# Kernel optimization log

Measured on AMD Instinct MI355X. Metric: run time of the kernel, lower is better.

The kernel has to match this reference:

```python
import jax, jax.numpy as jnp
import numpy as np

KSIZE = 20      # gaussian smoothing kernel size
SIGMA = 2.0     # gaussianSmoothWidth
STRIDE = 4      # strideLen
KLEN = 14       # kernelLen
LN_EPS = 1e-5


def _gauss_smooth(x):
    # x: [B, T, D]; depthwise conv1d along time, padding='same' (torch: left 9, right 10)
    D = x.shape[-1]
    i = jnp.arange(KSIZE, dtype=x.dtype)
    g = jnp.exp(-0.5 * ((i - (KSIZE - 1) / 2.0) / SIGMA) ** 2)
    g = g / jnp.sum(g)
    k = jnp.tile(g[None, None, :], (D, 1, 1))  # [D, 1, KSIZE]
    y = jax.lax.conv_general_dilated(
        jnp.swapaxes(x, 1, 2), k,
        window_strides=(1,), padding=[(9, 10)],
        feature_group_count=D,
        dimension_numbers=('NCW', 'OIW', 'NCW'))
    return jnp.swapaxes(y, 1, 2)


def _qrnn_layer(x, W, b):
    # SpeechBrain QuasiRNNLayer (output_gate=True, unidirectional, zoneout=0)
    # x: [B, T, F]; W: [3H, 2F]; b: [3H]
    xprev = jnp.concatenate([jnp.zeros_like(x[:, :1]), x[:, :-1]], axis=1)
    y = jnp.einsum('btf,gf->btg', jnp.concatenate([x, xprev], axis=-1), W) + b
    z, f, o = jnp.split(y, 3, axis=-1)
    z = jnp.tanh(z)
    f = jax.nn.sigmoid(f)
    fz = f * z
    # recurrence: c_t = f_t*z_t + (1-f_t)*c_{t-1}, c_0-input = 0
    def step(c, ins):
        f_t, fz_t = ins
        c = fz_t + (1.0 - f_t) * c
        return c, c
    c0 = jnp.zeros((f.shape[0], f.shape[2]), f.dtype)
    _, cs = jax.lax.scan(step, c0, (jnp.swapaxes(f, 0, 1), jnp.swapaxes(fz, 0, 1)))
    c = jnp.swapaxes(cs, 0, 1)  # [B, T, H]
    return jax.nn.sigmoid(o) * c


def reference(neuralInput, dayWeights, dayBias, w0, b0, w_rest, b_rest,
              ln_gamma, ln_beta, w_out, b_out, dayIdx):
    x = _gauss_smooth(neuralInput)                    # [B, T, D]
    Wd = dayWeights[dayIdx]                           # [B, D, D]
    bd = dayBias[dayIdx]                              # [B, 1, D]
    x = jnp.einsum('btd,bdk->btk', x, Wd) + bd
    x = x / (1.0 + jnp.abs(x))                        # Softsign
    B, T, D = x.shape
    Tp = (T - KLEN) // STRIDE + 1
    idx = jnp.arange(Tp)[:, None] * STRIDE + jnp.arange(KLEN)[None, :]
    win = x[:, idx, :]                                # [B, Tp, K, D]
    # torch Unfold ordering: channel-major -> feature index = d*KLEN + k
    strided = jnp.transpose(win, (0, 1, 3, 2)).reshape(B, Tp, D * KLEN)
    h = _qrnn_layer(strided, w0, b0)
    for i in range(w_rest.shape[0]):
        h = _qrnn_layer(h, w_rest[i], b_rest[i])
    mu = jnp.mean(h, axis=-1, keepdims=True)
    var = jnp.mean(jnp.square(h - mu), axis=-1, keepdims=True)
    hn = (h - mu) * jax.lax.rsqrt(var + LN_EPS) * ln_gamma + ln_beta
    return jnp.einsum('bth,ch->btc', hn, w_out) + b_out


def setup_inputs() -> dict:
    key = jax.random.key(0)
    ks = jax.random.split(key, 10)
    B, T, D, H, L, NDAYS, C = 32, 2000, 256, 512, 3, 24, 41
    F0 = D * KLEN  # 3584
    inp = {}
    inp['neuralInput'] = jax.random.normal(ks[0], (B, T, D), jnp.float32)
    inp['dayIdx'] = jax.random.randint(ks[1], (B,), 0, NDAYS, jnp.int64 if jax.config.jax_enable_x64 else jnp.int32)
    eye = jnp.eye(D, dtype=jnp.float32)
    inp['dayWeights'] = eye[None] + 0.02 * jax.random.normal(ks[2], (NDAYS, D, D), jnp.float32)
    inp['dayBias'] = jnp.zeros((NDAYS, 1, D), jnp.float32)
    inp['w0'] = jax.random.normal(ks[3], (3 * H, 2 * F0), jnp.float32) / np.sqrt(2 * F0)
    inp['b0'] = jnp.zeros((3 * H,), jnp.float32)
    inp['w_rest'] = jax.random.normal(ks[4], (L - 1, 3 * H, 2 * H), jnp.float32) / np.sqrt(2 * H)
    inp['b_rest'] = jnp.zeros((L - 1, 3 * H), jnp.float32)
    inp['ln_gamma'] = jnp.ones((H,), jnp.float32)
    inp['ln_beta'] = jnp.zeros((H,), jnp.float32)
    inp['w_out'] = jax.random.normal(ks[5], (C, H), jnp.float32) / np.sqrt(H)
    inp['b_out'] = jnp.zeros((C,), jnp.float32)
    return inp
```

## Files before the change

kernel.cpp:

```cpp
#include <hip/hip_runtime.h>
#include <hip/hip_bf16.h>

typedef __hip_bfloat16 bf16;
typedef __attribute__((ext_vector_type(8))) short bf16x8;
typedef __attribute__((ext_vector_type(4))) float f32x4;

__device__ __forceinline__ float fsig(float x) { return 1.f / (1.f + __expf(-x)); }
__device__ __forceinline__ float ftanh(float x) { return 1.f - 2.f / (1.f + __expf(2.f * x)); }
__device__ __forceinline__ float b2f(short s) {
  union { float f; unsigned u; } x;
  x.u = ((unsigned)(unsigned short)s) << 16;
  return x.f;
}

#define GT 16
__global__ __launch_bounds__(256) void gauss_kernel(const float* __restrict__ X,
                                                    bf16* __restrict__ Y, int T) {
  int b = blockIdx.y, t0 = blockIdx.x * GT;
  int tid = threadIdx.x;
  __shared__ float xs[GT + 19][256];
  const float* xb = X + (long)b * T * 256;
  for (int r = 0; r < GT + 19; ++r) {
    int tt = t0 + r - 9;
    xs[r][tid] = (tt >= 0 && tt < T) ? xb[(long)tt * 256 + tid] : 0.f;
  }
  __syncthreads();
  float g[20];
  float norm = 0.f;
#pragma unroll
  for (int j = 0; j < 20; ++j) {
    float u = (j - 9.5f) * 0.5f;
    g[j] = expf(-0.5f * u * u);
    norm += g[j];
  }
  float rn = 1.f / norm;
  for (int i = 0; i < GT; ++i) {
    int t = t0 + i;
    if (t >= T) break;
    float acc = 0.f;
#pragma unroll
    for (int j = 0; j < 20; ++j) acc += g[j] * xs[i + j][tid];
    Y[((long)b * T + t) * 256 + tid] = (bf16)(acc * rn);
  }
}

__global__ __launch_bounds__(256) void transpose_day(const float* __restrict__ W,
                                                     bf16* __restrict__ Wt) {
  __shared__ float tile[64][65];
  int d0 = blockIdx.x * 64, g0 = blockIdx.y * 64, day = blockIdx.z;
  const float* Wd = W + (long)day * 65536;
  int tx = threadIdx.x & 63, ty = threadIdx.x >> 6;
  for (int i = 0; i < 16; ++i) {
    int d = ty + i * 4;
    tile[d][tx] = Wd[(long)(d0 + d) * 256 + g0 + tx];
  }
  __syncthreads();
  bf16* outp = Wt + (((long)day * 4 + (d0 >> 6)) * 256 + g0) * 64;
  for (int i = 0; i < 16; ++i) {
    int g = ty + i * 4;
    outp[(long)g * 64 + tx] = (bf16)tile[tx][g];
  }
}

__global__ void prep_misc(const float* __restrict__ w0, const float* __restrict__ w_rest,
                          const float* __restrict__ w_out,
                          bf16* __restrict__ V2, bf16* __restrict__ wrb2,
                          bf16* __restrict__ w0b, bf16* __restrict__ h1s,
                          bf16* __restrict__ h2s, bf16* __restrict__ zpage,
                          bf16* __restrict__ wo_bf) {
  long i = (long)blockIdx.x * 256 + threadIdx.x;
  if (i < 7077888L) {
    int u = (int)(i / (1536 * 256));
    int r = (int)(i % (1536 * 256));
    int g = r >> 8, d = r & 255;
    float v = 0.f;
    if (u < 14) v += w0[(long)g * 7168 + 3584 + d * 14 + u];
    if (u >= 4) v += w0[(long)g * 7168 + d * 14 + (u - 4)];
    V2[(((long)u * 4 + (d >> 6)) * 1536 + g) * 64 + (d & 63)] = (bf16)v;
    return;
  }
  i -= 7077888L;
  if (i < 3145728L) {
    int L = (int)(i / (1536 * 1024));
    int r = (int)(i % (1536 * 1024));
    int g = r >> 10, k = r & 1023;
    float v = w_rest[(long)L * 1536 * 1024 + (long)g * 1024 + (k ^ 512)];
    wrb2[(long)L * 16 * 1536 * 64 + ((long)(k >> 6) * 1536 + g) * 64 + (k & 63)] = (bf16)v;
    return;
  }
  i -= 3145728L;
  if (i < 5505024L) {
    long g = i / 3584;
    int j = (int)(i - g * 3584);
    w0b[i] = (bf16)w0[g * 7168 + j];
    return;
  }
  i -= 5505024L;
  if (i < 16384) {
    int b = (int)(i >> 9), k = (int)(i & 511);
    h1s[(long)b * 498 * 512 + k] = (bf16)0.f;
    h2s[(long)b * 498 * 512 + k] = (bf16)0.f;
    return;
  }
  i -= 16384;
  if (i < 128) { zpage[i] = (bf16)0.f; return; }
  i -= 128;
  if (i < 20992) wo_bf[i] = (bf16)w_out[i];
}

__global__ __launch_bounds__(256, 4) void mfma97(
    const bf16* __restrict__ A, const bf16* __restrict__ W,
    const float* __restrict__ bias, bf16* __restrict__ Y,
    const int* __restrict__ dayIdx, const bf16* __restrict__ zpage,
    long astride, int Ta, int rstride, int Tm, int N, int tstride,
    int ntaps, int nch, int tap_off0, int NW, long dayWStride,
    int dayBStride, int mode, int nti, int ngi) {
  __shared__ __align__(16) char smem[32768];
  const int id = blockIdx.x;
  const int bi = id / (ngi * nti);
  const int rem = id - bi * (ngi * nti);
  const int gi = rem / nti;
  const int ti = rem - gi * nti;
  const int g0 = gi * 128, t0 = ti * 128;

  const bf16* Ab = A + (long)bi * astride;
  long wbase = 0;
  int boff = 0;
  if (dayIdx) {
    int di = dayIdx[bi];
    wbase = (long)di * dayWStride;
    boff = di * dayBStride;
  }
  const int tid = threadIdx.x;
  const int lane = tid & 63;
  const int w = tid >> 6;
  const int wm = (w >> 1) * 64, wn = (w & 1) * 64;
  const int lr = lane & 15, lg = lane >> 4;

  f32x4 acc[4][4] = {};

  for (int tap = 0; tap < ntaps; ++tap) {
    for (int dblk = 0; dblk < nch; ++dblk) {
      int d0 = dblk << 6;
      int s = tap * nch + dblk;
      const bf16* Wp = W + wbase + ((long)s * NW + g0) * 64;
#pragma unroll
      for (int j = 0; j < 8; ++j) {
        int q = j * 256 + tid;
        int qw = j * 256 + w * 64;
        const bf16* src;
        if (j < 4) {
          int row = q >> 3;
          int u = (q & 7) ^ (row & 7);
          int time = (t0 + row) * tstride + tap + tap_off0;
          src = (time >= 0 && time < Ta) ? Ab + (long)time * rstride + d0 + u * 8
                                         : zpage;
        } else {
          int row = (q >> 3) - 128;
          int u = (q & 7) ^ (row & 7);
          src = Wp + row * 64 + u * 8;
        }
        auto lp = (__attribute__((address_space(3))) void*)(smem + qw * 16);
        __builtin_amdgcn_global_load_lds(
            (const __attribute__((address_space(1))) void*)src, lp, 16, 0, 0);
      }
      __syncthreads();
#pragma unroll
      for (int kc = 0; kc < 2; ++kc) {
        int ub = kc * 4 + lg;
        bf16x8 af[4], bw[4];
#pragma unroll
        for (int f = 0; f < 4; ++f) {
          int m = wm + f * 16 + lr;
          af[f] = *reinterpret_cast<const bf16x8*>(smem + m * 128 + ((ub ^ (m & 7)) << 4));
          int g = wn + f * 16 + lr;
          bw[f] = *reinterpret_cast<const bf16x8*>(smem + 16384 + g * 128 +
                                                   ((ub ^ (g & 7)) << 4));
        }
#pragma unroll
        for (int fm = 0; fm < 4; ++fm)
#pragma unroll
          for (int fn = 0; fn < 4; ++fn)
            acc[fm][fn] = __builtin_amdgcn_mfma_f32_16x16x32_bf16(af[fm], bw[fn],
                                                                  acc[fm][fn], 0, 0, 0);
      }
      __syncthreads();
    }
  }
#pragma unroll
  for (int fn = 0; fn < 4; ++fn) {
    int gcol = g0 + wn + fn * 16 + lr;
    float bb = bias[boff + gcol];
    int sect = gcol >> 9;
#pragma unroll
    for (int fm = 0; fm < 4; ++fm) {
#pragma unroll
      for (int rr = 0; rr < 4; ++rr) {
        int t = t0 + wm + fm * 16 + lg * 4 + rr;
        if (t >= Tm) continue;
        float v = acc[fm][fn][rr] + bb;
        float e;
        if (mode == 1) e = v / (1.f + fabsf(v));
        else e = (sect == 0) ? ftanh(v) : fsig(v);
        Y[((long)bi * Tm + t) * N + gcol] = (bf16)e;
      }
    }
  }
}

__global__ void build_A0(const bf16* __restrict__ xs, bf16* __restrict__ A0) {
  int idx = blockIdx.x * 256 + threadIdx.x;
  if (idx >= 32 * 3584) return;
  int b = idx / 3584, j = idx % 3584;
  int d = j / 14, u = j % 14;
  A0[idx] = xs[((long)b * 2000 + u) * 256 + d];
}

__global__ __launch_bounds__(256) void t0_gemm(const bf16* __restrict__ A0,
                                               const bf16* __restrict__ W0b,
                                               float* __restrict__ part) {
  int g0 = blockIdx.x * 128;
  int ks = blockIdx.y;
  int k0 = ks * 512;
  __shared__ __align__(16) bf16 Wl[128 * 64];
  __shared__ __align__(16) bf16 Alds[32 * 64];
  int tid = threadIdx.x;
  int lane = tid & 63, wave = tid >> 6;
  int wn = wave * 32;
  int lr = lane & 15, lg = lane >> 4;
  int srow = tid >> 3, su = tid & 7;
  f32x4 acc[2][2] = {};
  for (int c = 0; c < 8; ++c) {
    int d0 = k0 + c * 64;
#pragma unroll
    for (int i = 0; i < 4; ++i) {
      int m = srow + i * 32;
      *reinterpret_cast<bf16x8*>(&Wl[m * 64 + ((su ^ (m & 7)) << 3)]) =
          *reinterpret_cast<const bf16x8*>(W0b + (long)(g0 + m) * 3584 + d0 + su * 8);
    }
    {
      int m = srow;
      *reinterpret_cast<bf16x8*>(&Alds[m * 64 + ((su ^ (m & 7)) << 3)]) =
          *reinterpret_cast<const bf16x8*>(A0 + (long)m * 3584 + d0 + su * 8);
    }
    __syncthreads();
#pragma unroll
    for (int kc = 0; kc < 2; ++kc) {
      int ub = kc * 4 + lg;
      bf16x8 am[2], bwv[2];
#pragma unroll
      for (int f = 0; f < 2; ++f) {
        int m = f * 16 + lr;
        am[f] = *reinterpret_cast<const bf16x8*>(&Alds[m * 64 + ((ub ^ (m & 7)) << 3)]);
        int g = wn + f * 16 + lr;
        bwv[f] = *reinterpret_cast<const bf16x8*>(&Wl[g * 64 + ((ub ^ (g & 7)) << 3)]);
      }
#pragma unroll
      for (int fm = 0; fm < 2; ++fm)
#pragma unroll
        for (int fn = 0; fn < 2; ++fn)
          acc[fm][fn] = __builtin_amdgcn_mfma_f32_16x16x32_bf16(am[fm], bwv[fn],
                                                                acc[fm][fn], 0, 0, 0);
    }
    __syncthreads();
  }
#pragma unroll
  for (int fn = 0; fn < 2; ++fn) {
    int gcol = g0 + wn + fn * 16 + lr;
#pragma unroll
    for (int fm = 0; fm < 2; ++fm)
#pragma unroll
      for (int r = 0; r < 4; ++r) {
        int brow = fm * 16 + lg * 4 + r;
        part[((long)ks * 32 + brow) * 1536 + gcol] = acc[fm][fn][r];
      }
  }
}

__global__ void t0_reduce(const float* __restrict__ part, const float* __restrict__ b0,
                          bf16* __restrict__ yact, int Tp) {
  int idx = blockIdx.x * 256 + threadIdx.x;
  if (idx >= 32 * 1536) return;
  int b = idx / 1536, g = idx % 1536;
  float s = b0[g];
#pragma unroll
  for (int k = 0; k < 7; ++k) s += part[((long)k * 32 + b) * 1536 + g];
  float e = (g < 512) ? ftanh(s) : fsig(s);
  yact[(long)b * Tp * 1536 + g] = (bf16)e;
}

#define NC 8
#define LC 63
__global__ __launch_bounds__(256) void scan_pass1(const bf16* __restrict__ Yv,
                                                  float* __restrict__ Afac,
                                                  float* __restrict__ Bfac, int Tp) {
  int idx = blockIdx.x * 256 + threadIdx.x;
  int ci = idx >> 14;
  int chain = idx & 16383;
  int b = chain >> 9, hh = chain & 511;
  const bf16* yb = Yv + (long)b * Tp * 1536 + hh;
  int t0 = ci * LC, t1 = min(t0 + LC, Tp);
  float A = 1.f, Bv = 0.f;
  for (int t = t0; t < t1; ++t) {
    const bf16* p = yb + (long)t * 1536;
    float zt = (float)p[0], fs = (float)p[512];
    Bv = fs * zt + (1.f - fs) * Bv;
    A *= (1.f - fs);
  }
  Afac[idx] = A;
  Bfac[idx] = Bv;
}

__global__ __launch_bounds__(256) void scan_pass3(const bf16* __restrict__ Yv,
                                                  const float* __restrict__ Afac,
                                                  const float* __restrict__ Bfac,
                                                  bf16* __restrict__ H, int Tp) {
  int idx = blockIdx.x * 256 + threadIdx.x;
  int ci = idx >> 14;
  int chain = idx & 16383;
  int b = chain >> 9, hh = chain & 511;
  const bf16* yb = Yv + (long)b * Tp * 1536 + hh;
  bf16* hb = H + ((long)b * 498 + 1) * 512 + hh;
  float c = 0.f;
  for (int k = 0; k < ci; ++k)
    c = Afac[k * 16384 + chain] * c + Bfac[k * 16384 + chain];
  int t0 = ci * LC, t1 = min(t0 + LC, Tp);
  for (int t = t0; t < t1; ++t) {
    const bf16* p = yb + (long)t * 1536;
    float zt = (float)p[0], fs = (float)p[512], so = (float)p[1024];
    c = fs * zt + (1.f - fs) * c;
    hb[(long)t * 512] = (bf16)(so * c);
  }
}

#define TS 8
__global__ __launch_bounds__(256) void ln_out_kernel(
    const bf16* __restrict__ Hs, const float* __restrict__ gamma,
    const float* __restrict__ beta, const bf16* __restrict__ WoBf,
    const float* __restrict__ bo, float* __restrict__ Out) {
  __shared__ bf16 wol[41 * 512];
  __shared__ float hl[512];
  __shared__ float rs[4], rs2[4];
  int tid = threadIdx.x;
  int wid = tid >> 6, lane = tid & 63;
  for (int i = tid; i < 41 * 512 / 8; i += 256)
    reinterpret_cast<bf16x8*>(wol)[i] = reinterpret_cast<const bf16x8*>(WoBf)[i];
  __syncthreads();
  long base = (long)blockIdx.x * TS;
  for (int r = 0; r < TS; ++r) {
    long bt = base + r;
    if (bt >= 32L * 497) break;
    int b = (int)(bt / 497), t = (int)(bt % 497);
    const bf16* hrow = Hs + ((long)b * 498 + 1 + t) * 512;
    float v0 = (float)hrow[tid], v1 = (float)hrow[tid + 256];
    float s = v0 + v1, s2 = v0 * v0 + v1 * v1;
#pragma unroll
    for (int d = 32; d; d >>= 1) {
      s += __shfl_down(s, d);
      s2 += __shfl_down(s2, d);
    }
    if (lane == 0) {
      rs[wid] = s;
      rs2[wid] = s2;
    }
    __syncthreads();
    float sum = rs[0] + rs[1] + rs[2] + rs[3];
    float sum2 = rs2[0] + rs2[1] + rs2[2] + rs2[3];
    float mu = sum * (1.f / 512.f);
    float var = sum2 * (1.f / 512.f) - mu * mu;
    float rstd = rsqrtf(var + 1e-5f);
    hl[tid] = (v0 - mu) * rstd * gamma[tid] + beta[tid];
    hl[tid + 256] = (v1 - mu) * rstd * gamma[tid + 256] + beta[tid + 256];
    __syncthreads();
    const float4* hp = reinterpret_cast<const float4*>(&hl[lane * 8]);
    float4 h0v = hp[0], h1v = hp[1];
    for (int c = wid; c < 41; c += 4) {
      bf16x8 w0v = *reinterpret_cast<const bf16x8*>(&wol[c * 512 + lane * 8]);
      float a = b2f(w0v[0]) * h0v.x + b2f(w0v[1]) * h0v.y +
                b2f(w0v[2]) * h0v.z + b2f(w0v[3]) * h0v.w +
                b2f(w0v[4]) * h1v.x + b2f(w0v[5]) * h1v.y +
                b2f(w0v[6]) * h1v.z + b2f(w0v[7]) * h1v.w;
#pragma unroll
      for (int d = 32; d; d >>= 1) a += __shfl_down(a, d);
      if (lane == 0) Out[bt * 41 + c] = a + bo[c];
    }
    __syncthreads();
  }
}

extern "C" void kernel_launch(void* const* d_in, const int* in_sizes, int n_in,
                              void* d_out, int out_size, void* d_ws, size_t ws_size,
                              hipStream_t stream) {
  const float* neuralInput = (const float*)d_in[0];
  const int* dayIdx = (const int*)d_in[1];
  const float* dayWeights = (const float*)d_in[2];
  const float* dayBias = (const float*)d_in[3];
  const float* w0 = (const float*)d_in[4];
  const float* b0 = (const float*)d_in[5];
  const float* w_rest = (const float*)d_in[6];
  const float* b_rest = (const float*)d_in[7];
  const float* ln_gamma = (const float*)d_in[8];
  const float* ln_beta = (const float*)d_in[9];
  const float* w_out = (const float*)d_in[10];
  const float* b_out = (const float*)d_in[11];
  float* out = (float*)d_out;

  const int B = 32, T = 2000, Tp = 497;

  char* p = (char*)d_ws;
  bf16* yact = (bf16*)p;  p += 48857088;
  bf16* xs0b = (bf16*)p;  p += 32768000;
  bf16* xs = (bf16*)p;    p += 32768000;
  bf16* V2 = (bf16*)p;    p += 14155776;
  bf16* dWb2 = (bf16*)p;  p += 3145728;
  bf16* wrb2 = (bf16*)p;  p += 6291456;
  bf16* w0b = (bf16*)p;   p += 11010048;
  bf16* A0 = (bf16*)p;    p += 229376;
  float* part = (float*)p; p += 1376256;
  bf16* h1s = (bf16*)p;   p += 16320512;
  bf16* h2s = (bf16*)p;   p += 16320512;
  float* Afac = (float*)p; p += 524288;
  float* Bfac = (float*)p; p += 524288;
  bf16* zpage = (bf16*)p;  p += 256;
  bf16* wo_bf = (bf16*)p;  p += 42240;

  hipLaunchKernelGGL(prep_misc, dim3((15766272L + 255) / 256), dim3(256), 0, stream,
                     w0, w_rest, w_out, V2, wrb2, w0b, h1s, h2s, zpage, wo_bf);
  hipLaunchKernelGGL(transpose_day, dim3(4, 4, 24), dim3(256), 0, stream, dayWeights, dWb2);
  hipLaunchKernelGGL(gauss_kernel, dim3((T + GT - 1) / GT, B), dim3(256), 0, stream,
                     neuralInput, xs0b, T);
  hipLaunchKernelGGL(mfma97, dim3(1024), dim3(256), 0, stream, xs0b, dWb2, dayBias,
                     xs, dayIdx, zpage, (long)T * 256, T, 256, T, 256, 1, 1, 4, 0,
                     256, 65536L, 256, 1, 16, 2);
  hipLaunchKernelGGL(build_A0, dim3((32 * 3584 + 255) / 256), dim3(256), 0, stream, xs, A0);
  hipLaunchKernelGGL(t0_gemm, dim3(12, 7), dim3(256), 0, stream, A0, w0b, part);
  hipLaunchKernelGGL(mfma97, dim3(1536), dim3(256), 0, stream, xs, V2, b0, yact,
                     (const int*)nullptr, zpage, (long)T * 256, T, 256, Tp, 1536, 4,
                     18, 4, -4, 1536, 0L, 0, 2, 4, 12);
  hipLaunchKernelGGL(t0_reduce, dim3((32 * 1536 + 255) / 256), dim3(256), 0, stream,
                     part, b0, yact, Tp);
  hipLaunchKernelGGL(scan_pass1, dim3(512), dim3(256), 0, stream, yact, Afac, Bfac, Tp);
  hipLaunchKernelGGL(scan_pass3, dim3(512), dim3(256), 0, stream, yact, Afac, Bfac, h1s, Tp);
  for (int i = 0; i < 2; ++i) {
    bf16* hin = (i == 0) ? h1s : h2s;
    bf16* hout = (i == 0) ? h2s : h1s;
    hipLaunchKernelGGL(mfma97, dim3(1536), dim3(256), 0, stream, hin,
                       wrb2 + (long)i * 16 * 1536 * 64, b_rest + (long)i * 1536, yact,
                       (const int*)nullptr, zpage, 498L * 512, Tp, 512, Tp, 1536, 1,
                       1, 16, 0, 1536, 0L, 0, 2, 4, 12);
    hipLaunchKernelGGL(scan_pass1, dim3(512), dim3(256), 0, stream, yact, Afac, Bfac, Tp);
    hipLaunchKernelGGL(scan_pass3, dim3(512), dim3(256), 0, stream, yact, Afac, Bfac, hout, Tp);
  }
  hipLaunchKernelGGL(ln_out_kernel, dim3((32 * 497 + TS - 1) / TS), dim3(256), 0, stream,
                     h1s, ln_gamma, ln_beta, wo_bf, b_out, out);
}
```

Before: 868.5 us.

## Stage w0 rows in shared memory, enlarge gauss tile, batch-fastest block order

The w0 preprocessing moves into its own kernel, one block per output row. Each block stages its 7168-float row in LDS and writes both the bf16 copy and the tap-combined V2 layout from there, replacing strided gather reads from global memory. The gauss smoothing time tile grows from 16 to 32, which cuts the redundant halo loads per block. The mfma97 block index is remapped so the batch index varies fastest, meant to improve reuse of shared weight tiles across concurrently running blocks; this hardcodes a batch of 32.

Result: no change. 863.1 us (-0.6%).

```diff
diff --git a/kernel.cpp b/kernel.cpp
--- a/kernel.cpp
+++ b/kernel.cpp
@@ -13,7 +13,7 @@
   return x.f;
 }
 
-#define GT 16
+#define GT 32
 __global__ __launch_bounds__(256) void gauss_kernel(const float* __restrict__ X,
                                                     bf16* __restrict__ Y, int T) {
   int b = blockIdx.y, t0 = blockIdx.x * GT;
@@ -62,24 +62,30 @@
   }
 }
 
-__global__ void prep_misc(const float* __restrict__ w0, const float* __restrict__ w_rest,
-                          const float* __restrict__ w_out,
-                          bf16* __restrict__ V2, bf16* __restrict__ wrb2,
-                          bf16* __restrict__ w0b, bf16* __restrict__ h1s,
+__global__ __launch_bounds__(256) void prep_w0(const float* __restrict__ w0,
+                                               bf16* __restrict__ V2,
+                                               bf16* __restrict__ w0b) {
+  int g = blockIdx.x;
+  __shared__ float row[7168];
+  const float* src = w0 + (long)g * 7168;
+  for (int i = threadIdx.x; i < 7168; i += 256) row[i] = src[i];
+  __syncthreads();
+  bf16* wb = w0b + (long)g * 3584;
+  for (int i = threadIdx.x; i < 3584; i += 256) wb[i] = (bf16)row[i];
+  for (int i = threadIdx.x; i < 18 * 256; i += 256) {
+    int u = i >> 8, d = i & 255;
+    float v = 0.f;
+    if (u < 14) v += row[3584 + d * 14 + u];
+    if (u >= 4) v += row[d * 14 + (u - 4)];
+    V2[(((long)u * 4 + (d >> 6)) * 1536 + g) * 64 + (d & 63)] = (bf16)v;
+  }
+}
+
+__global__ void prep_rest(const float* __restrict__ w_rest, const float* __restrict__ w_out,
+                          bf16* __restrict__ wrb2, bf16* __restrict__ h1s,
                           bf16* __restrict__ h2s, bf16* __restrict__ zpage,
                           bf16* __restrict__ wo_bf) {
   long i = (long)blockIdx.x * 256 + threadIdx.x;
-  if (i < 7077888L) {
-    int u = (int)(i / (1536 * 256));
-    int r = (int)(i % (1536 * 256));
-    int g = r >> 8, d = r & 255;
-    float v = 0.f;
-    if (u < 14) v += w0[(long)g * 7168 + 3584 + d * 14 + u];
-    if (u >= 4) v += w0[(long)g * 7168 + d * 14 + (u - 4)];
-    V2[(((long)u * 4 + (d >> 6)) * 1536 + g) * 64 + (d & 63)] = (bf16)v;
-    return;
-  }
-  i -= 7077888L;
   if (i < 3145728L) {
     int L = (int)(i / (1536 * 1024));
     int r = (int)(i % (1536 * 1024));
@@ -89,13 +95,6 @@
     return;
   }
   i -= 3145728L;
-  if (i < 5505024L) {
-    long g = i / 3584;
-    int j = (int)(i - g * 3584);
-    w0b[i] = (bf16)w0[g * 7168 + j];
-    return;
-  }
-  i -= 5505024L;
   if (i < 16384) {
     int b = (int)(i >> 9), k = (int)(i & 511);
     h1s[(long)b * 498 * 512 + k] = (bf16)0.f;
@@ -117,8 +116,8 @@
     int dayBStride, int mode, int nti, int ngi) {
   __shared__ __align__(16) char smem[32768];
   const int id = blockIdx.x;
-  const int bi = id / (ngi * nti);
-  const int rem = id - bi * (ngi * nti);
+  const int bi = id & 31;
+  const int rem = id >> 5;
   const int gi = rem / nti;
   const int ti = rem - gi * nti;
   const int g0 = gi * 128, t0 = ti * 128;
@@ -424,8 +423,9 @@
   bf16* zpage = (bf16*)p;  p += 256;
   bf16* wo_bf = (bf16*)p;  p += 42240;
 
-  hipLaunchKernelGGL(prep_misc, dim3((15766272L + 255) / 256), dim3(256), 0, stream,
-                     w0, w_rest, w_out, V2, wrb2, w0b, h1s, h2s, zpage, wo_bf);
+  hipLaunchKernelGGL(prep_rest, dim3((3183232L + 255) / 256), dim3(256), 0, stream,
+                     w_rest, w_out, wrb2, h1s, h2s, zpage, wo_bf);
+  hipLaunchKernelGGL(prep_w0, dim3(1536), dim3(256), 0, stream, w0, V2, w0b);
   hipLaunchKernelGGL(transpose_day, dim3(4, 4, 24), dim3(256), 0, stream, dayWeights, dWb2);
   hipLaunchKernelGGL(gauss_kernel, dim3((T + GT - 1) / GT, B), dim3(256), 0, stream,
                      neuralInput, xs0b, T);
```
